# Performance work log

Measured on AMD Instinct MI355X. Metric: run time of the kernel, lower is better.

Reference implementation:

```python
import jax, jax.numpy as jnp
import numpy as np

DEPTH, HEADS, DIM, DH = 6, 3, 3, 128
INNER = HEADS * DH            # 384
M = int(DH * np.log(DH))      # 620 random features (performer_pytorch default)
FF = 4 * DIM                  # 12
EPS = 1e-4


def setup_inputs() -> dict:
    key = jax.random.key(0)
    ks = jax.random.split(key, 12)
    B, N = 8, 4096
    s = 0.1
    return {
        "x": jax.random.normal(ks[0], (B, N, DIM), jnp.float32),
        "Wq": jax.random.normal(ks[1], (DEPTH, DIM, INNER), jnp.float32) * s,
        "Wk": jax.random.normal(ks[2], (DEPTH, DIM, INNER), jnp.float32) * s,
        "Wv": jax.random.normal(ks[3], (DEPTH, DIM, INNER), jnp.float32) * s,
        "Wo": jax.random.normal(ks[4], (DEPTH, INNER, DIM), jnp.float32) * s,
        "bo": jnp.zeros((DEPTH, DIM), jnp.float32),
        "ln1_g": jnp.ones((DEPTH, DIM), jnp.float32),
        "ln1_b": jnp.zeros((DEPTH, DIM), jnp.float32),
        "W1": jax.random.normal(ks[5], (DEPTH, DIM, FF), jnp.float32) * s,
        "b1": jnp.zeros((DEPTH, FF), jnp.float32),
        "W2": jax.random.normal(ks[6], (DEPTH, FF, DIM), jnp.float32) * s,
        "b2": jnp.zeros((DEPTH, DIM), jnp.float32),
        "ln2_g": jnp.ones((DEPTH, DIM), jnp.float32),
        "ln2_b": jnp.zeros((DEPTH, DIM), jnp.float32),
        "proj": jax.random.normal(ks[7], (DEPTH, M, DH), jnp.float32),
        "dec_w": jax.random.normal(ks[8], (DIM, 1), jnp.float32) * s,
        "dec_b": jnp.zeros((1,), jnp.float32),
    }


def layernorm(x, g, b):
    mu = x.mean(-1, keepdims=True)
    var = ((x - mu) ** 2).mean(-1, keepdims=True)
    return (x - mu) * jax.lax.rsqrt(var + 1e-5) * g + b


def softmax_kernel(data, proj, is_query):
    # data: [b,h,n,dh], proj: [m,dh] -> positive random features [b,h,n,m]
    dn = DH ** -0.25                    # data normalizer 1/sqrt(sqrt(d))
    ratio = M ** -0.5
    dd = jnp.einsum('bhnd,md->bhnm', data * dn, proj)
    diag = 0.5 * (dn ** 2) * (data ** 2).sum(-1, keepdims=True)  # [b,h,n,1]
    if is_query:
        mx = jnp.max(dd, axis=-1, keepdims=True)
    else:
        mx = jnp.max(dd, axis=(-1, -2), keepdims=True)
    return ratio * (jnp.exp(dd - diag - mx) + EPS)


def favor_attention(x, Wq, Wk, Wv, Wo, bo, proj):
    b, n, _ = x.shape
    split = lambda t: t.reshape(b, n, HEADS, DH).transpose(0, 2, 1, 3)
    q, k, v = split(x @ Wq), split(x @ Wk), split(x @ Wv)   # [b,h,n,dh]
    qp = softmax_kernel(q, proj, True)    # [b,h,n,m]
    kp = softmax_kernel(k, proj, False)
    k_sum = kp.sum(axis=2)                                   # [b,h,m]
    d_inv = 1.0 / jnp.einsum('bhnm,bhm->bhn', qp, k_sum)
    ctx = jnp.einsum('bhnm,bhnd->bhmd', kp, v)               # [b,h,m,dh]
    out = jnp.einsum('bhnm,bhmd,bhn->bhnd', qp, ctx, d_inv)
    out = out.transpose(0, 2, 1, 3).reshape(b, n, INNER)
    return out @ Wo + bo


def reference(x, Wq, Wk, Wv, Wo, bo, ln1_g, ln1_b, W1, b1, W2, b2, ln2_g, ln2_b, proj, dec_w, dec_b):
    for i in range(DEPTH):
        h = layernorm(x, ln1_g[i], ln1_b[i])
        x = x + favor_attention(h, Wq[i], Wk[i], Wv[i], Wo[i], bo[i], proj[i])
        h = layernorm(x, ln2_g[i], ln2_b[i])
        x = x + (jax.nn.gelu(h @ W1[i] + b1[i], approximate=False) @ W2[i] + b2[i])
    return jax.nn.sigmoid(x @ dec_w + dec_b)
```

## Files before the change

kernel.cpp:

```cpp
#include <hip/hip_runtime.h>
#include <math.h>

#define B_ 8
#define N_ 4096
#define H_ 3
#define DH_ 128
#define INNER_ 384
#define M_ 620
#define MP_ 640
#define DEPTH_ 6
#define BH_ 24

static constexpr float DN_ = 0.29730177875068026f;
static constexpr float RATIO_ = 0.04016096644512494f;
static constexpr float EPS_ = 1e-4f;

typedef __attribute__((ext_vector_type(8))) short short8;
typedef __attribute__((ext_vector_type(4))) float f32x4;

__device__ __forceinline__ short f2bf(float f) {
  union { float f; unsigned u; } x; x.f = f;
  unsigned r = x.u + 0x7FFF + ((x.u >> 16) & 1);
  return (short)(r >> 16);
}
__device__ __forceinline__ float bf2f(short s) {
  union { unsigned u; float f; } x; x.u = ((unsigned)(unsigned short)s) << 16;
  return x.f;
}
__device__ __forceinline__ float4 ldg4(const float* p) { return *(const float4*)p; }

__device__ __forceinline__ unsigned cvtpk(float lo, float hi) {
  unsigned r;
  asm("v_cvt_pk_bf16_f32 %0, %1, %2" : "=v"(r) : "v"(lo), "v"(hi));
  return r;
}

__device__ __forceinline__ void gl2lds(const void* g, void* l) {
  __builtin_amdgcn_global_load_lds(
      (const __attribute__((address_space(1))) void*)g,
      (__attribute__((address_space(3))) void*)l, 16, 0, 0);
}

__device__ __forceinline__ void stage_t256(const char* gbase, char* lds, int w, int l) {
  int row = w * 4 + (l >> 4);
  int col = ((l & 15) * 16) ^ ((row & 7) << 4);
  char* lp = lds + __builtin_amdgcn_readfirstlane(w << 10);
  gl2lds(gbase + row * 256 + col, lp);
}

__device__ __forceinline__ void stage_t64(const char* gbase, size_t growb, char* lds,
                                          int w, int l) {
  int d = w * 16 + (l >> 2);
  int swl = ((((l >> 2) ^ (l >> 4)) & 3) << 4);
  int col = ((l & 3) * 16) ^ swl;
  char* lp = lds + __builtin_amdgcn_readfirstlane(w << 10);
  gl2lds(gbase + (size_t)d * growb + col, lp);
}

__global__ void k_copy(const float* __restrict__ s, float* __restrict__ d, int n) {
  int i = blockIdx.x * 256 + threadIdx.x;
  if (i < n) d[i] = s[i];
}

__global__ void k_projcvt(const float* __restrict__ proj, short* __restrict__ pb) {
  int i = blockIdx.x * 256 + threadIdx.x;
  if (i >= DEPTH_ * MP_ * DH_) return;
  int l = i / (MP_ * DH_);
  int rem = i - l * (MP_ * DH_);
  int m = rem >> 7, d = rem & 127;
  pb[i] = (m < M_) ? f2bf(proj[((size_t)l * M_ + m) * DH_ + d]) : (short)0;
}

__global__ __launch_bounds__(384) void k_ln_qkv(
    const float* __restrict__ x, const float* __restrict__ Wq,
    const float* __restrict__ Wk, const float* __restrict__ Wv,
    const float* __restrict__ g1, const float* __restrict__ b1,
    short* __restrict__ qb, short* __restrict__ kb, short* __restrict__ vtp) {
  __shared__ float xs[96];
  int c = threadIdx.x;
  int token0 = blockIdx.x * 32;
  int b = token0 >> 12, n0 = token0 & 4095;
  if (c < 96) xs[c] = x[(size_t)token0 * 3 + c];
  float wq0 = Wq[c], wq1 = Wq[INNER_ + c], wq2 = Wq[2 * INNER_ + c];
  float wk0 = Wk[c], wk1 = Wk[INNER_ + c], wk2 = Wk[2 * INNER_ + c];
  float wv0 = Wv[c], wv1 = Wv[INNER_ + c], wv2 = Wv[2 * INNER_ + c];
  float G0 = g1[0], G1 = g1[1], G2 = g1[2];
  float B0 = b1[0], B1 = b1[1], B2 = b1[2];
  int hh = c >> 7, dh = c & 127;
  size_t rowbase = ((size_t)(b * H_ + hh) * N_ + n0) * DH_ + dh;
  __syncthreads();
  short8 v8[4];
#pragma unroll
  for (int tt = 0; tt < 32; ++tt) {
    float x0 = xs[tt * 3], x1 = xs[tt * 3 + 1], x2 = xs[tt * 3 + 2];
    float mu = (x0 + x1 + x2) * (1.f / 3.f);
    float d0 = x0 - mu, d1 = x1 - mu, d2 = x2 - mu;
    float rs = rsqrtf((d0 * d0 + d1 * d1 + d2 * d2) * (1.f / 3.f) + 1e-5f);
    float h0 = d0 * rs * G0 + B0;
    float h1 = d1 * rs * G1 + B1;
    float h2 = d2 * rs * G2 + B2;
    qb[rowbase + (size_t)tt * DH_] = f2bf((h0 * wq0 + h1 * wq1 + h2 * wq2) * DN_);
    kb[rowbase + (size_t)tt * DH_] = f2bf((h0 * wk0 + h1 * wk1 + h2 * wk2) * DN_);
    const int p = ((tt >> 2) & 3) * 8 + ((tt >> 4) & 1) * 4 + (tt & 3);
    v8[p >> 3][p & 7] = f2bf(h0 * wv0 + h1 * wv1 + h2 * wv2);
  }
  short* dst = vtp + ((size_t)(b * H_ + hh) * DH_ + dh) * N_ + n0;
  *(short8*)dst = v8[0];
  *(short8*)(dst + 8) = v8[1];
  *(short8*)(dst + 16) = v8[2];
  *(short8*)(dst + 24) = v8[3];
}

__global__ __launch_bounds__(256) void k_diag(const short* __restrict__ kb,
                                              float* __restrict__ diag_k) {
  int nt = blockIdx.x, bh = blockIdx.y;
  int t = threadIdx.x;
  int n = t >> 3, seg = t & 7;
  const short* src = kb + ((size_t)bh * N_ + nt * 32 + n) * DH_ + seg * 16;
  short8 a = *(const short8*)src;
  short8 b2 = *(const short8*)(src + 8);
  float s = 0.f;
#pragma unroll
  for (int j = 0; j < 8; ++j) {
    float va = bf2f(a[j]), vb = bf2f(b2[j]);
    s = fmaf(va, va, s);
    s = fmaf(vb, vb, s);
  }
  s += __shfl_down(s, 4);
  s += __shfl_down(s, 2);
  s += __shfl_down(s, 1);
  if (seg == 0) diag_k[(size_t)bh * N_ + nt * 32 + n] = 0.5f * s;
}

__global__ __launch_bounds__(512) void k_kp_ctx(
    const short* __restrict__ kb, const short* __restrict__ vtp,
    const short* __restrict__ pb, const float* __restrict__ diag_k,
    float* __restrict__ Cpart, float* __restrict__ spart,
    float* __restrict__ bmx) {
  int ns = blockIdx.x, mt = blockIdx.y, bh = blockIdx.z;
  __shared__ __align__(16) char Ks[2][8192];
  __shared__ __align__(16) char Vts[2][8192];
  __shared__ float diag_s[1024];
  int t = threadIdx.x, w = t >> 6, l = t & 63, lr = l & 15, lg = l >> 4;
  {
    const float* dbase = diag_k + (size_t)bh * N_ + ns * 1024;
#pragma unroll
    for (int i = 0; i < 2; ++i) diag_s[t + i * 512] = dbase[t + i * 512];
  }
  int m0 = mt * 128 + w * 16;
  short8 bfr[4];
  {
    const short* pr = pb + (size_t)(m0 + lr) * DH_ + lg * 8;
#pragma unroll
    for (int ks = 0; ks < 4; ++ks) bfr[ks] = *(const short8*)(pr + ks * 32);
  }
  const char* kgb = (const char*)(kb + ((size_t)bh * N_ + ns * 1024) * DH_);
  const char* vgb = (const char*)(vtp + (size_t)bh * DH_ * N_ + ns * 1024);
  stage_t256(kgb, Ks[0], w, l);
  stage_t64(vgb, (size_t)N_ * 2, Vts[0], w, l);
  __syncthreads();
  f32x4 cacc[8];
#pragma unroll
  for (int db = 0; db < 8; ++db) cacc[db] = (f32x4){0.f, 0.f, 0.f, 0.f};
  float ksacc = 0.f;
  float bm = -INFINITY;
  const bool mv = (m0 + lr) < M_;
  int xk = (lr & 7) << 4;
  int xv = ((lr ^ (lr >> 2)) & 3) << 4;
  for (int ch = 0; ch < 32; ++ch) {
    int cur = ch & 1;
    if (ch < 31) {
      stage_t256(kgb + (size_t)(ch + 1) * 32 * 256, Ks[cur ^ 1], w, l);
      stage_t64(vgb + (size_t)(ch + 1) * 64, (size_t)N_ * 2, Vts[cur ^ 1], w, l);
    }
    int n0 = ch * 32;
    f32x4 dd[2];
    __builtin_amdgcn_s_setprio(1);
#pragma unroll
    for (int nsub = 0; nsub < 2; ++nsub) {
      f32x4 acc = {0.f, 0.f, 0.f, 0.f};
#pragma unroll
      for (int ks = 0; ks < 4; ++ks)
        acc = __builtin_amdgcn_mfma_f32_16x16x32_bf16(
            *(const short8*)(Ks[cur] + (nsub * 16 + lr) * 256 +
                             ((lg * 16 + ks * 64) ^ xk)),
            bfr[ks], acc, 0, 0, 0);
      dd[nsub] = acc;
    }
    __builtin_amdgcn_s_setprio(0);
    float cm = -INFINITY;
    if (mv) {
#pragma unroll
      for (int nsub = 0; nsub < 2; ++nsub)
#pragma unroll
        for (int rg = 0; rg < 4; ++rg) cm = fmaxf(cm, dd[nsub][rg]);
    }
#pragma unroll
    for (int off = 1; off < 64; off <<= 1) cm = fmaxf(cm, __shfl_xor(cm, off));
    if (cm > bm) {
      float sc = __expf(bm - cm);
      bm = cm;
      ksacc *= sc;
#pragma unroll
      for (int db = 0; db < 8; ++db)
#pragma unroll
        for (int rg = 0; rg < 4; ++rg) cacc[db][rg] *= sc;
    }
    float ev[8];
#pragma unroll
    for (int nsub = 0; nsub < 2; ++nsub)
#pragma unroll
      for (int rg = 0; rg < 4; ++rg) {
        float e = __expf(dd[nsub][rg] - diag_s[n0 + nsub * 16 + 4 * lg + rg] - bm);
        ev[nsub * 4 + rg] = e;
        ksacc += e;
      }
    union { short8 s8; unsigned u[4]; } ea;
#pragma unroll
    for (int i = 0; i < 4; ++i) ea.u[i] = cvtpk(ev[2 * i], ev[2 * i + 1]);
    __builtin_amdgcn_s_setprio(1);
#pragma unroll
    for (int db = 0; db < 8; ++db)
      cacc[db] = __builtin_amdgcn_mfma_f32_16x16x32_bf16(
          ea.s8, *(const short8*)(Vts[cur] + (db * 16 + lr) * 64 + ((lg * 16) ^ xv)),
          cacc[db], 0, 0, 0);
    __builtin_amdgcn_s_setprio(0);
    __syncthreads();
  }
  float* Cp = Cpart + ((size_t)ns * BH_ + bh) * MP_ * DH_;
#pragma unroll
  for (int db = 0; db < 8; ++db) {
    int d = db * 16 + lr;
#pragma unroll
    for (int rg = 0; rg < 4; ++rg)
      Cp[(size_t)(m0 + 4 * lg + rg) * DH_ + d] = cacc[db][rg];
  }
  ksacc += __shfl_down(ksacc, 32);
  ksacc += __shfl_down(ksacc, 16);
  if (l < 16) spart[((size_t)ns * BH_ + bh) * MP_ + m0 + l] = ksacc;
  if (l == 0) bmx[((size_t)ns * BH_ + bh) * 40 + mt * 8 + w] = bm;
}

__global__ __launch_bounds__(256) void k_gmax(const float* __restrict__ bmx,
                                              float* __restrict__ mxk) {
  int bh = blockIdx.x, t = threadIdx.x;
  float v = -INFINITY;
  if (t < 160) {
    int ns = t / 40, g = t - ns * 40;
    v = bmx[((size_t)ns * BH_ + bh) * 40 + g];
  }
#pragma unroll
  for (int off = 32; off; off >>= 1) v = fmaxf(v, __shfl_xor(v, off));
  __shared__ float red[4];
  if ((t & 63) == 0) red[t >> 6] = v;
  __syncthreads();
  if (t == 0) mxk[bh] = fmaxf(fmaxf(red[0], red[1]), fmaxf(red[2], red[3]));
}

__global__ __launch_bounds__(256) void k_vsum(
    const short* __restrict__ vtp, float* __restrict__ vsp) {
  int d = blockIdx.x, bh = blockIdx.y, t = threadIdx.x;
  const short8* row = (const short8*)(vtp + ((size_t)bh * DH_ + d) * N_);
  short8 a = row[t * 2], b2 = row[t * 2 + 1];
  float s = 0.f;
#pragma unroll
  for (int j = 0; j < 8; ++j) s += bf2f(a[j]) + bf2f(b2[j]);
  __shared__ float red[256];
  red[t] = s;
  __syncthreads();
  for (int st = 128; st; st >>= 1) {
    if (t < st) red[t] += red[t + st];
    __syncthreads();
  }
  if (t == 0) vsp[bh * DH_ + d] = red[0];
}

__global__ __launch_bounds__(256) void k_fin_ctx(
    const float* __restrict__ Cpart, const float* __restrict__ vsp,
    const float* __restrict__ bmx, const float* __restrict__ mxk,
    short* __restrict__ ctxtp, float* __restrict__ cspart) {
  int mt = blockIdx.x, bh = blockIdx.y;
  __shared__ float vsv[128];
  __shared__ short tile[128][40];
  int t = threadIdx.x;
  if (t < 128) vsv[t] = vsp[bh * DH_ + t] * EPS_;
  __syncthreads();
  int r = t >> 3, seg = t & 7;
  int d0 = seg * 16;
  int m = mt * 32 + r;
  int p = ((r >> 2) & 3) * 8 + ((r >> 4) & 1) * 4 + (r & 3);
  const size_t ph = (size_t)BH_ * MP_ * DH_;
  const float* c0 = Cpart + (size_t)bh * MP_ * DH_ + (size_t)m * DH_ + d0;
  if (m < M_) {
    float mxg = mxk[bh];
    int g = m >> 4;
    float sc0 = __expf(bmx[((size_t)0 * BH_ + bh) * 40 + g] - mxg);
    float sc1 = __expf(bmx[((size_t)1 * BH_ + bh) * 40 + g] - mxg);
    float sc2 = __expf(bmx[((size_t)2 * BH_ + bh) * 40 + g] - mxg);
    float sc3 = __expf(bmx[((size_t)3 * BH_ + bh) * 40 + g] - mxg);
#pragma unroll
    for (int j4 = 0; j4 < 4; ++j4) {
      float4 a = ldg4(c0 + j4 * 4);
      float4 b = ldg4(c0 + ph + j4 * 4);
      float4 c = ldg4(c0 + 2 * ph + j4 * 4);
      float4 e = ldg4(c0 + 3 * ph + j4 * 4);
      float vals[4] = {sc0 * a.x + sc1 * b.x + sc2 * c.x + sc3 * e.x,
                       sc0 * a.y + sc1 * b.y + sc2 * c.y + sc3 * e.y,
                       sc0 * a.z + sc1 * b.z + sc2 * c.z + sc3 * e.z,
                       sc0 * a.w + sc1 * b.w + sc2 * c.w + sc3 * e.w};
#pragma unroll
      for (int j = 0; j < 4; ++j) {
        int d = d0 + j4 * 4 + j;
        tile[d][p] = f2bf(RATIO_ * (vals[j] + vsv[d]));
      }
    }
  } else {
#pragma unroll
    for (int j = 0; j < 16; ++j) tile[d0 + j][p] = 0;
  }
  __syncthreads();
  int d = t >> 1, half = t & 1;
  short* dst = ctxtp + ((size_t)bh * DH_ + d) * MP_ + mt * 32 + half * 16;
  short8 s0 = *(const short8*)&tile[d][half * 16];
  short8 s1 = *(const short8*)&tile[d][half * 16 + 8];
  *(short8*)dst = s0;
  *(short8*)(dst + 8) = s1;
  float cs = 0.f;
#pragma unroll
  for (int j = 0; j < 8; ++j) cs += bf2f(s0[j]) + bf2f(s1[j]);
  cs += __shfl_xor(cs, 1);
  if (half == 0) cspart[((size_t)bh * 20 + mt) * DH_ + d] = cs;
}

__global__ __launch_bounds__(128) void k_fin2(
    const float* __restrict__ cspart, const float* __restrict__ spart,
    const float* __restrict__ bmx, const float* __restrict__ mxk,
    float* __restrict__ ctxsum, short* __restrict__ ksum_pb,
    float* __restrict__ ksumtot) {
  int bh = blockIdx.x, d = threadIdx.x;
  float s = 0.f;
#pragma unroll
  for (int mt = 0; mt < 20; ++mt) s += cspart[((size_t)bh * 20 + mt) * DH_ + d];
  ctxsum[bh * DH_ + d] = s;
  float mxg = mxk[bh];
  __shared__ float red[128];
  float kt = 0.f;
  for (int m = d; m < MP_; m += 128) {
    float ks = 0.f;
    if (m < M_) {
      size_t o = (size_t)bh * MP_ + m;
      size_t sh = (size_t)BH_ * MP_;
      int g = m >> 4;
      float s0 = __expf(bmx[((size_t)0 * BH_ + bh) * 40 + g] - mxg);
      float s1 = __expf(bmx[((size_t)1 * BH_ + bh) * 40 + g] - mxg);
      float s2 = __expf(bmx[((size_t)2 * BH_ + bh) * 40 + g] - mxg);
      float s3 = __expf(bmx[((size_t)3 * BH_ + bh) * 40 + g] - mxg);
      ks = RATIO_ * (s0 * spart[o] + s1 * spart[o + sh] + s2 * spart[o + 2 * sh] +
                     s3 * spart[o + 3 * sh] + EPS_ * (float)N_);
    }
    int r = m & 31;
    int p = ((r >> 2) & 3) * 8 + ((r >> 4) & 1) * 4 + (r & 3);
    ksum_pb[(size_t)bh * MP_ + (m & ~31) + p] = f2bf(ks);
    kt += ks;
  }
  red[d] = kt;
  __syncthreads();
  for (int st = 64; st > 0; st >>= 1) {
    if (d < st) red[d] += red[d + st];
    __syncthreads();
  }
  if (d == 0) ksumtot[bh] = red[0];
}

__global__ __launch_bounds__(512) void k_q_attn(
    const short* __restrict__ qb, const short* __restrict__ pb,
    const short* __restrict__ ctxtp, const short* __restrict__ ksum_pb,
    const float* __restrict__ ctxsum, const float* __restrict__ ksumtot,
    float* __restrict__ o) {
  int nt = blockIdx.x, bh = blockIdx.y;
  __shared__ __align__(16) char Pj[2][8192];
  __shared__ __align__(16) char Ct[2][8192];
  __shared__ __align__(16) short kslp[MP_];
  int t = threadIdx.x, w = t >> 6, l = t & 63, lr = l & 15, lg = l >> 4;
  if (t < MP_ / 8)
    ((short8*)kslp)[t] = ((const short8*)(ksum_pb + (size_t)bh * MP_))[t];
  const short* qr = qb + ((size_t)bh * N_ + nt * 128 + w * 16 + lr) * DH_ + lg * 8;
  short8 qfr[4];
#pragma unroll
  for (int ks = 0; ks < 4; ++ks) qfr[ks] = *(const short8*)(qr + ks * 32);
  float dq;
  {
    float s2 = 0.f;
#pragma unroll
    for (int ks = 0; ks < 4; ++ks)
#pragma unroll
      for (int j = 0; j < 8; ++j) {
        float v = bf2f(qfr[ks][j]);
        s2 = fmaf(v, v, s2);
      }
    s2 += __shfl_xor(s2, 16);
    s2 += __shfl_xor(s2, 32);
    dq = 0.5f * s2;
  }
  const char* cgb = (const char*)(ctxtp + (size_t)bh * DH_ * MP_);
  stage_t256((const char*)pb, Pj[0], w, l);
  stage_t64(cgb, (size_t)MP_ * 2, Ct[0], w, l);
  __syncthreads();
  f32x4 cacc[8];
#pragma unroll
  for (int db = 0; db < 8; ++db) cacc[db] = (f32x4){0.f, 0.f, 0.f, 0.f};
  f32x4 dacc = {0.f, 0.f, 0.f, 0.f};
  float om = -INFINITY;
  int xk = (lr & 7) << 4;
  int xv = ((lr ^ (lr >> 2)) & 3) << 4;
  for (int mc = 0; mc < 20; ++mc) {
    int cur = mc & 1;
    if (mc < 19) {
      stage_t256((const char*)(pb + (size_t)(mc + 1) * 32 * DH_), Pj[cur ^ 1], w, l);
      stage_t64(cgb + (size_t)(mc + 1) * 64, (size_t)MP_ * 2, Ct[cur ^ 1], w, l);
    }
    int m0 = mc * 32;
    f32x4 qk[2];
    __builtin_amdgcn_s_setprio(1);
#pragma unroll
    for (int ms = 0; ms < 2; ++ms) {
      f32x4 acc = {0.f, 0.f, 0.f, 0.f};
#pragma unroll
      for (int ks = 0; ks < 4; ++ks)
        acc = __builtin_amdgcn_mfma_f32_16x16x32_bf16(
            *(const short8*)(Pj[cur] + (ms * 16 + lr) * 256 +
                             ((lg * 16 + ks * 64) ^ xk)),
            qfr[ks], acc, 0, 0, 0);
      qk[ms] = acc;
    }
    __builtin_amdgcn_s_setprio(0);
    float cm = -INFINITY;
#pragma unroll
    for (int ms = 0; ms < 2; ++ms)
#pragma unroll
      for (int rg = 0; rg < 4; ++rg) {
        int mg = m0 + ms * 16 + 4 * lg + rg;
        if (mg < M_) cm = fmaxf(cm, qk[ms][rg]);
      }
    cm = fmaxf(cm, __shfl_xor(cm, 16));
    cm = fmaxf(cm, __shfl_xor(cm, 32));
    if (__any(cm > om)) {
      float nm = fmaxf(om, cm);
      float sc = __expf(om - nm);
      om = nm;
      float scr[4];
#pragma unroll
      for (int rg = 0; rg < 4; ++rg) scr[rg] = __shfl(sc, 4 * lg + rg);
#pragma unroll
      for (int rg = 0; rg < 4; ++rg) dacc[rg] *= scr[rg];
#pragma unroll
      for (int db = 0; db < 8; ++db)
#pragma unroll
        for (int rg = 0; rg < 4; ++rg) cacc[db][rg] *= scr[rg];
    }
    float dqm = dq + om;
    float ev[8];
#pragma unroll
    for (int ms = 0; ms < 2; ++ms)
#pragma unroll
      for (int rg = 0; rg < 4; ++rg)
        ev[ms * 4 + rg] = __expf(qk[ms][rg] - dqm);
    union { short8 s8; unsigned u[4]; } ea;
#pragma unroll
    for (int i = 0; i < 4; ++i) ea.u[i] = cvtpk(ev[2 * i], ev[2 * i + 1]);
    __builtin_amdgcn_s_setprio(1);
    dacc = __builtin_amdgcn_mfma_f32_16x16x32_bf16(
        ea.s8, *(const short8*)&kslp[m0 + lg * 8], dacc, 0, 0, 0);
#pragma unroll
    for (int db = 0; db < 8; ++db)
      cacc[db] = __builtin_amdgcn_mfma_f32_16x16x32_bf16(
          ea.s8, *(const short8*)(Ct[cur] + (db * 16 + lr) * 64 + ((lg * 16) ^ xv)),
          cacc[db], 0, 0, 0);
    __builtin_amdgcn_s_setprio(0);
    __syncthreads();
  }
  float kst = ksumtot[bh];
  float dinv[4];
#pragma unroll
  for (int rg = 0; rg < 4; ++rg)
    dinv[rg] = 1.f / (RATIO_ * (dacc[rg] + EPS_ * kst));
  float* ob = o + ((size_t)bh * N_ + nt * 128 + w * 16) * DH_;
#pragma unroll
  for (int db = 0; db < 8; ++db) {
    int d = db * 16 + lr;
    float cs = ctxsum[bh * DH_ + d] * EPS_;
#pragma unroll
    for (int rg = 0; rg < 4; ++rg)
      ob[(size_t)(4 * lg + rg) * DH_ + d] = RATIO_ * (cacc[db][rg] + cs) * dinv[rg];
  }
}

__global__ __launch_bounds__(256) void k_wo_ffn(
    const float* __restrict__ attn, const float* __restrict__ Wo,
    const float* __restrict__ bo, const float* __restrict__ g2,
    const float* __restrict__ be2, const float* __restrict__ W1,
    const float* __restrict__ bf1, const float* __restrict__ W2,
    const float* __restrict__ bf2, float* __restrict__ x) {
  __shared__ float wols[INNER_ * 3];
  __shared__ float bos[3];
  __shared__ float acc3[4][8][3];
  int t = threadIdx.x;
  for (int i = t; i < INNER_ * 3; i += 256) wols[i] = Wo[i];
  if (t < 3) bos[t] = bo[t];
  __syncthreads();
  int w = t >> 6, l = t & 63;
  int base = (blockIdx.x * 4 + w) * 8;
#pragma unroll
  for (int tt = 0; tt < 8; ++tt) {
    int token = base + tt;
    int b = token >> 12, n = token & 4095;
    float p0 = 0.f, p1 = 0.f, p2 = 0.f;
#pragma unroll
    for (int s = 0; s < 6; ++s) {
      int inner = l + 64 * s;
      int h = inner >> 7, dh = inner & 127;
      float a = attn[(((size_t)(b * H_ + h)) * N_ + n) * DH_ + dh];
      p0 = fmaf(a, wols[inner * 3 + 0], p0);
      p1 = fmaf(a, wols[inner * 3 + 1], p1);
      p2 = fmaf(a, wols[inner * 3 + 2], p2);
    }
#pragma unroll
    for (int off = 32; off; off >>= 1) {
      p0 += __shfl_down(p0, off);
      p1 += __shfl_down(p1, off);
      p2 += __shfl_down(p2, off);
    }
    if (l == 0) {
      acc3[w][tt][0] = p0 + bos[0];
      acc3[w][tt][1] = p1 + bos[1];
      acc3[w][tt][2] = p2 + bos[2];
    }
  }
  __syncthreads();
  if (l < 8) {
    int token = base + l;
    float x0 = x[(size_t)token * 3 + 0] + acc3[w][l][0];
    float x1 = x[(size_t)token * 3 + 1] + acc3[w][l][1];
    float x2 = x[(size_t)token * 3 + 2] + acc3[w][l][2];
    float mu = (x0 + x1 + x2) * (1.f / 3.f);
    float d0 = x0 - mu, d1 = x1 - mu, d2 = x2 - mu;
    float rs = rsqrtf((d0 * d0 + d1 * d1 + d2 * d2) * (1.f / 3.f) + 1e-5f);
    float h0 = d0 * rs * g2[0] + be2[0];
    float h1 = d1 * rs * g2[1] + be2[1];
    float h2 = d2 * rs * g2[2] + be2[2];
    float y0 = x0 + bf2[0], y1 = x1 + bf2[1], y2 = x2 + bf2[2];
#pragma unroll
    for (int tt = 0; tt < 12; ++tt) {
      float f = h0 * W1[tt] + h1 * W1[12 + tt] + h2 * W1[24 + tt] + bf1[tt];
      float g = 0.5f * f * (1.f + erff(f * 0.70710678118654752f));
      y0 += g * W2[tt * 3 + 0];
      y1 += g * W2[tt * 3 + 1];
      y2 += g * W2[tt * 3 + 2];
    }
    x[(size_t)token * 3 + 0] = y0;
    x[(size_t)token * 3 + 1] = y1;
    x[(size_t)token * 3 + 2] = y2;
  }
}

__global__ void k_decode(const float* __restrict__ x, const float* __restrict__ dw,
                         const float* __restrict__ db, float* __restrict__ out) {
  int t = blockIdx.x * 256 + threadIdx.x;
  if (t < B_ * N_) {
    float l = x[(size_t)t * 3 + 0] * dw[0] + x[(size_t)t * 3 + 1] * dw[1] +
              x[(size_t)t * 3 + 2] * dw[2] + db[0];
    out[t] = 1.f / (1.f + expf(-l));
  }
}

extern "C" void kernel_launch(void* const* d_in, const int* in_sizes, int n_in,
                              void* d_out, int out_size, void* d_ws, size_t ws_size,
                              hipStream_t stream) {
  const float* x_in = (const float*)d_in[0];
  const float* Wq = (const float*)d_in[1];
  const float* Wk = (const float*)d_in[2];
  const float* Wv = (const float*)d_in[3];
  const float* Wo = (const float*)d_in[4];
  const float* bo = (const float*)d_in[5];
  const float* ln1g = (const float*)d_in[6];
  const float* ln1b = (const float*)d_in[7];
  const float* W1 = (const float*)d_in[8];
  const float* b1 = (const float*)d_in[9];
  const float* W2 = (const float*)d_in[10];
  const float* b2 = (const float*)d_in[11];
  const float* ln2g = (const float*)d_in[12];
  const float* ln2b = (const float*)d_in[13];
  const float* proj = (const float*)d_in[14];
  const float* dec_w = (const float*)d_in[15];
  const float* dec_b = (const float*)d_in[16];

  const size_t XB = (size_t)B_ * N_ * 3;
  const size_t QKV = (size_t)BH_ * N_ * DH_;
  const size_t CTX = (size_t)BH_ * MP_ * DH_;
  const size_t SS = (size_t)BH_ * MP_;

  char* p = (char*)d_ws;
  auto alloc = [&](size_t bytes) {
    char* r = p;
    p += (bytes + 255) & ~(size_t)255;
    return r;
  };
  float* xbuf = (float*)alloc(XB * 4);
  short* qb = (short*)alloc(QKV * 2);
  short* kb = (short*)alloc(QKV * 2);
  float* diag_k = (float*)alloc((size_t)BH_ * N_ * 4);
  short* pb = (short*)alloc((size_t)DEPTH_ * MP_ * DH_ * 2);
  short* vtp = (short*)alloc(QKV * 2);
  short* ctxtp = (short*)alloc(CTX * 2);
  float* o = (float*)alloc(QKV * 4);
  float* Cpart = o;
  float* spart = (float*)alloc(4 * SS * 4);
  float* cspart = (float*)alloc((size_t)BH_ * 20 * DH_ * 4);
  short* ksum_pb = (short*)alloc(SS * 2);
  float* vsp = (float*)alloc((size_t)BH_ * DH_ * 4);
  float* ctxsum = (float*)alloc((size_t)BH_ * DH_ * 4);
  float* ksumtot = (float*)alloc(BH_ * 4);
  float* bmx = (float*)alloc((size_t)4 * BH_ * 40 * 4);
  float* mxk = (float*)alloc(BH_ * 4);

  k_copy<<<(XB + 255) / 256, 256, 0, stream>>>(x_in, xbuf, (int)XB);
  k_projcvt<<<(DEPTH_ * MP_ * DH_ + 255) / 256, 256, 0, stream>>>(proj, pb);

  for (int i = 0; i < DEPTH_; ++i) {
    const short* pbL = pb + (size_t)i * MP_ * DH_;
    k_ln_qkv<<<B_ * N_ / 32, 384, 0, stream>>>(xbuf, Wq + (size_t)i * 3 * INNER_,
                                               Wk + (size_t)i * 3 * INNER_,
                                               Wv + (size_t)i * 3 * INNER_,
                                               ln1g + i * 3, ln1b + i * 3,
                                               qb, kb, vtp);
    k_diag<<<dim3(N_ / 32, BH_), 256, 0, stream>>>(kb, diag_k);
    k_kp_ctx<<<dim3(4, 5, BH_), 512, 0, stream>>>(kb, vtp, pbL, diag_k,
                                                  Cpart, spart, bmx);
    k_vsum<<<dim3(DH_, BH_), 256, 0, stream>>>(vtp, vsp);
    k_gmax<<<BH_, 256, 0, stream>>>(bmx, mxk);
    k_fin_ctx<<<dim3(20, BH_), 256, 0, stream>>>(Cpart, vsp, bmx, mxk,
                                                 ctxtp, cspart);
    k_fin2<<<BH_, 128, 0, stream>>>(cspart, spart, bmx, mxk,
                                    ctxsum, ksum_pb, ksumtot);
    k_q_attn<<<dim3(32, BH_), 512, 0, stream>>>(qb, pbL, ctxtp, ksum_pb,
                                                ctxsum, ksumtot, o);
    k_wo_ffn<<<B_ * N_ / 32, 256, 0, stream>>>(o, Wo + (size_t)i * INNER_ * 3,
                                               bo + i * 3, ln2g + i * 3, ln2b + i * 3,
                                               W1 + (size_t)i * 36, b1 + (size_t)i * 12,
                                               W2 + (size_t)i * 36, b2 + i * 3, xbuf);
  }
  k_decode<<<(B_ * N_ + 255) / 256, 256, 0, stream>>>(xbuf, dec_w, dec_b, (float*)d_out);
}
```

Before: 1.075 ms.

## Merge diag/vsum kernels, fold gmax into finalizers, double k_kp_ctx stage size

Merges the k_diag and k_vsum kernels into one launch that branches on blockIdx. The k_gmax kernel is removed and its per-head max reduction is recomputed inside both k_fin_ctx and k_fin2. k_kp_ctx now stages 64 rows per pipeline step instead of 32, halving the number of barriers and loop iterations at the cost of twice the shared memory (about 68KB), which may reduce occupancy. The main aim is to cut launch overhead and synchronisation across six layers.

New measurement: 1.044 ms. 1.03x faster.

```diff
diff --git a/kernel.cpp b/kernel.cpp
--- a/kernel.cpp
+++ b/kernel.cpp
@@ -111,25 +111,43 @@
   *(short8*)(dst + 24) = v8[3];
 }
 
-__global__ __launch_bounds__(256) void k_diag(const short* __restrict__ kb,
-                                              float* __restrict__ diag_k) {
-  int nt = blockIdx.x, bh = blockIdx.y;
-  int t = threadIdx.x;
-  int n = t >> 3, seg = t & 7;
-  const short* src = kb + ((size_t)bh * N_ + nt * 32 + n) * DH_ + seg * 16;
-  short8 a = *(const short8*)src;
-  short8 b2 = *(const short8*)(src + 8);
-  float s = 0.f;
-#pragma unroll
-  for (int j = 0; j < 8; ++j) {
-    float va = bf2f(a[j]), vb = bf2f(b2[j]);
-    s = fmaf(va, va, s);
-    s = fmaf(vb, vb, s);
-  }
-  s += __shfl_down(s, 4);
-  s += __shfl_down(s, 2);
-  s += __shfl_down(s, 1);
-  if (seg == 0) diag_k[(size_t)bh * N_ + nt * 32 + n] = 0.5f * s;
+__global__ __launch_bounds__(256) void k_dv(
+    const short* __restrict__ kb, const short* __restrict__ vtp,
+    float* __restrict__ diag_k, float* __restrict__ vsp) {
+  __shared__ float red[256];
+  int xx = blockIdx.x, bh = blockIdx.y, t = threadIdx.x;
+  if (xx < 128) {
+    int d = xx;
+    const short8* row = (const short8*)(vtp + ((size_t)bh * DH_ + d) * N_);
+    short8 a = row[t * 2], b2 = row[t * 2 + 1];
+    float s = 0.f;
+#pragma unroll
+    for (int j = 0; j < 8; ++j) s += bf2f(a[j]) + bf2f(b2[j]);
+    red[t] = s;
+    __syncthreads();
+    for (int st = 128; st; st >>= 1) {
+      if (t < st) red[t] += red[t + st];
+      __syncthreads();
+    }
+    if (t == 0) vsp[bh * DH_ + d] = red[0];
+  } else {
+    int nt = xx - 128;
+    int n = t >> 3, seg = t & 7;
+    const short* src = kb + ((size_t)bh * N_ + nt * 32 + n) * DH_ + seg * 16;
+    short8 a = *(const short8*)src;
+    short8 b2 = *(const short8*)(src + 8);
+    float s = 0.f;
+#pragma unroll
+    for (int j = 0; j < 8; ++j) {
+      float va = bf2f(a[j]), vb = bf2f(b2[j]);
+      s = fmaf(va, va, s);
+      s = fmaf(vb, vb, s);
+    }
+    s += __shfl_down(s, 4);
+    s += __shfl_down(s, 2);
+    s += __shfl_down(s, 1);
+    if (seg == 0) diag_k[(size_t)bh * N_ + nt * 32 + n] = 0.5f * s;
+  }
 }
 
 __global__ __launch_bounds__(512) void k_kp_ctx(
@@ -138,8 +156,8 @@
     float* __restrict__ Cpart, float* __restrict__ spart,
     float* __restrict__ bmx) {
   int ns = blockIdx.x, mt = blockIdx.y, bh = blockIdx.z;
-  __shared__ __align__(16) char Ks[2][8192];
-  __shared__ __align__(16) char Vts[2][8192];
+  __shared__ __align__(16) char Ks[2][16384];
+  __shared__ __align__(16) char Vts[2][16384];
   __shared__ float diag_s[1024];
   int t = threadIdx.x, w = t >> 6, l = t & 63, lr = l & 15, lg = l >> 4;
   {
@@ -157,7 +175,9 @@
   const char* kgb = (const char*)(kb + ((size_t)bh * N_ + ns * 1024) * DH_);
   const char* vgb = (const char*)(vtp + (size_t)bh * DH_ * N_ + ns * 1024);
   stage_t256(kgb, Ks[0], w, l);
+  stage_t256(kgb + 32 * 256, Ks[0] + 8192, w, l);
   stage_t64(vgb, (size_t)N_ * 2, Vts[0], w, l);
+  stage_t64(vgb + 64, (size_t)N_ * 2, Vts[0] + 8192, w, l);
   __syncthreads();
   f32x4 cacc[8];
 #pragma unroll
@@ -167,64 +187,73 @@
   const bool mv = (m0 + lr) < M_;
   int xk = (lr & 7) << 4;
   int xv = ((lr ^ (lr >> 2)) & 3) << 4;
-  for (int ch = 0; ch < 32; ++ch) {
-    int cur = ch & 1;
-    if (ch < 31) {
-      stage_t256(kgb + (size_t)(ch + 1) * 32 * 256, Ks[cur ^ 1], w, l);
-      stage_t64(vgb + (size_t)(ch + 1) * 64, (size_t)N_ * 2, Vts[cur ^ 1], w, l);
-    }
-    int n0 = ch * 32;
-    f32x4 dd[2];
-    __builtin_amdgcn_s_setprio(1);
-#pragma unroll
-    for (int nsub = 0; nsub < 2; ++nsub) {
-      f32x4 acc = {0.f, 0.f, 0.f, 0.f};
-#pragma unroll
-      for (int ks = 0; ks < 4; ++ks)
-        acc = __builtin_amdgcn_mfma_f32_16x16x32_bf16(
-            *(const short8*)(Ks[cur] + (nsub * 16 + lr) * 256 +
-                             ((lg * 16 + ks * 64) ^ xk)),
-            bfr[ks], acc, 0, 0, 0);
-      dd[nsub] = acc;
-    }
-    __builtin_amdgcn_s_setprio(0);
-    float cm = -INFINITY;
-    if (mv) {
+  for (int pc = 0; pc < 16; ++pc) {
+    int cur = pc & 1;
+    if (pc < 15) {
+      const char* kc = kgb + (size_t)(2 * pc + 2) * 32 * 256;
+      stage_t256(kc, Ks[cur ^ 1], w, l);
+      stage_t256(kc + 32 * 256, Ks[cur ^ 1] + 8192, w, l);
+      const char* vc = vgb + (size_t)(2 * pc + 2) * 64;
+      stage_t64(vc, (size_t)N_ * 2, Vts[cur ^ 1], w, l);
+      stage_t64(vc + 64, (size_t)N_ * 2, Vts[cur ^ 1] + 8192, w, l);
+    }
+#pragma unroll
+    for (int sub = 0; sub < 2; ++sub) {
+      const char* KS = Ks[cur] + sub * 8192;
+      const char* VS = Vts[cur] + sub * 8192;
+      int n0 = (2 * pc + sub) * 32;
+      f32x4 dd[2];
+      __builtin_amdgcn_s_setprio(1);
+#pragma unroll
+      for (int nsub = 0; nsub < 2; ++nsub) {
+        f32x4 acc = {0.f, 0.f, 0.f, 0.f};
+#pragma unroll
+        for (int ks = 0; ks < 4; ++ks)
+          acc = __builtin_amdgcn_mfma_f32_16x16x32_bf16(
+              *(const short8*)(KS + (nsub * 16 + lr) * 256 +
+                               ((lg * 16 + ks * 64) ^ xk)),
+              bfr[ks], acc, 0, 0, 0);
+        dd[nsub] = acc;
+      }
+      __builtin_amdgcn_s_setprio(0);
+      float cm = -INFINITY;
+      if (mv) {
+#pragma unroll
+        for (int nsub = 0; nsub < 2; ++nsub)
+#pragma unroll
+          for (int rg = 0; rg < 4; ++rg) cm = fmaxf(cm, dd[nsub][rg]);
+      }
+#pragma unroll
+      for (int off = 1; off < 64; off <<= 1) cm = fmaxf(cm, __shfl_xor(cm, off));
+      if (cm > bm) {
+        float sc = __expf(bm - cm);
+        bm = cm;
+        ksacc *= sc;
+#pragma unroll
+        for (int db = 0; db < 8; ++db)
+#pragma unroll
+          for (int rg = 0; rg < 4; ++rg) cacc[db][rg] *= sc;
+      }
+      float ev[8];
 #pragma unroll
       for (int nsub = 0; nsub < 2; ++nsub)
 #pragma unroll
-        for (int rg = 0; rg < 4; ++rg) cm = fmaxf(cm, dd[nsub][rg]);
-    }
-#pragma unroll
-    for (int off = 1; off < 64; off <<= 1) cm = fmaxf(cm, __shfl_xor(cm, off));
-    if (cm > bm) {
-      float sc = __expf(bm - cm);
-      bm = cm;
-      ksacc *= sc;
+        for (int rg = 0; rg < 4; ++rg) {
+          float e = __expf(dd[nsub][rg] - diag_s[n0 + nsub * 16 + 4 * lg + rg] - bm);
+          ev[nsub * 4 + rg] = e;
+          ksacc += e;
+        }
+      union { short8 s8; unsigned u[4]; } ea;
+#pragma unroll
+      for (int i = 0; i < 4; ++i) ea.u[i] = cvtpk(ev[2 * i], ev[2 * i + 1]);
+      __builtin_amdgcn_s_setprio(1);
 #pragma unroll
       for (int db = 0; db < 8; ++db)
-#pragma unroll
-        for (int rg = 0; rg < 4; ++rg) cacc[db][rg] *= sc;
-    }
-    float ev[8];
-#pragma unroll
-    for (int nsub = 0; nsub < 2; ++nsub)
-#pragma unroll
-      for (int rg = 0; rg < 4; ++rg) {
-        float e = __expf(dd[nsub][rg] - diag_s[n0 + nsub * 16 + 4 * lg + rg] - bm);
-        ev[nsub * 4 + rg] = e;
-        ksacc += e;
-      }
-    union { short8 s8; unsigned u[4]; } ea;
-#pragma unroll
-    for (int i = 0; i < 4; ++i) ea.u[i] = cvtpk(ev[2 * i], ev[2 * i + 1]);
-    __builtin_amdgcn_s_setprio(1);
-#pragma unroll
-    for (int db = 0; db < 8; ++db)
-      cacc[db] = __builtin_amdgcn_mfma_f32_16x16x32_bf16(
-          ea.s8, *(const short8*)(Vts[cur] + (db * 16 + lr) * 64 + ((lg * 16) ^ xv)),
-          cacc[db], 0, 0, 0);
-    __builtin_amdgcn_s_setprio(0);
+        cacc[db] = __builtin_amdgcn_mfma_f32_16x16x32_bf16(
+            ea.s8, *(const short8*)(VS + (db * 16 + lr) * 64 + ((lg * 16) ^ xv)),
+            cacc[db], 0, 0, 0);
+      __builtin_amdgcn_s_setprio(0);
+    }
     __syncthreads();
   }
   float* Cp = Cpart + ((size_t)ns * BH_ + bh) * MP_ * DH_;
@@ -241,50 +270,26 @@
   if (l == 0) bmx[((size_t)ns * BH_ + bh) * 40 + mt * 8 + w] = bm;
 }
 
-__global__ __launch_bounds__(256) void k_gmax(const float* __restrict__ bmx,
-                                              float* __restrict__ mxk) {
-  int bh = blockIdx.x, t = threadIdx.x;
-  float v = -INFINITY;
-  if (t < 160) {
-    int ns = t / 40, g = t - ns * 40;
-    v = bmx[((size_t)ns * BH_ + bh) * 40 + g];
-  }
-#pragma unroll
-  for (int off = 32; off; off >>= 1) v = fmaxf(v, __shfl_xor(v, off));
-  __shared__ float red[4];
-  if ((t & 63) == 0) red[t >> 6] = v;
-  __syncthreads();
-  if (t == 0) mxk[bh] = fmaxf(fmaxf(red[0], red[1]), fmaxf(red[2], red[3]));
-}
-
-__global__ __launch_bounds__(256) void k_vsum(
-    const short* __restrict__ vtp, float* __restrict__ vsp) {
-  int d = blockIdx.x, bh = blockIdx.y, t = threadIdx.x;
-  const short8* row = (const short8*)(vtp + ((size_t)bh * DH_ + d) * N_);
-  short8 a = row[t * 2], b2 = row[t * 2 + 1];
-  float s = 0.f;
-#pragma unroll
-  for (int j = 0; j < 8; ++j) s += bf2f(a[j]) + bf2f(b2[j]);
-  __shared__ float red[256];
-  red[t] = s;
-  __syncthreads();
-  for (int st = 128; st; st >>= 1) {
-    if (t < st) red[t] += red[t + st];
-    __syncthreads();
-  }
-  if (t == 0) vsp[bh * DH_ + d] = red[0];
-}
-
 __global__ __launch_bounds__(256) void k_fin_ctx(
     const float* __restrict__ Cpart, const float* __restrict__ vsp,
-    const float* __restrict__ bmx, const float* __restrict__ mxk,
+    const float* __restrict__ bmx,
     short* __restrict__ ctxtp, float* __restrict__ cspart) {
   int mt = blockIdx.x, bh = blockIdx.y;
   __shared__ float vsv[128];
   __shared__ short tile[128][40];
+  __shared__ float redm[4];
   int t = threadIdx.x;
   if (t < 128) vsv[t] = vsp[bh * DH_ + t] * EPS_;
-  __syncthreads();
+  float v = -INFINITY;
+  if (t < 160) {
+    int nsg = t / 40, g = t - nsg * 40;
+    v = bmx[((size_t)nsg * BH_ + bh) * 40 + g];
+  }
+#pragma unroll
+  for (int off = 32; off; off >>= 1) v = fmaxf(v, __shfl_xor(v, off));
+  if ((t & 63) == 0) redm[t >> 6] = v;
+  __syncthreads();
+  float mxg = fmaxf(fmaxf(redm[0], redm[1]), fmaxf(redm[2], redm[3]));
   int r = t >> 3, seg = t & 7;
   int d0 = seg * 16;
   int m = mt * 32 + r;
@@ -292,7 +297,6 @@
   const size_t ph = (size_t)BH_ * MP_ * DH_;
   const float* c0 = Cpart + (size_t)bh * MP_ * DH_ + (size_t)m * DH_ + d0;
   if (m < M_) {
-    float mxg = mxk[bh];
     int g = m >> 4;
     float sc0 = __expf(bmx[((size_t)0 * BH_ + bh) * 40 + g] - mxg);
     float sc1 = __expf(bmx[((size_t)1 * BH_ + bh) * 40 + g] - mxg);
@@ -334,15 +338,25 @@
 
 __global__ __launch_bounds__(128) void k_fin2(
     const float* __restrict__ cspart, const float* __restrict__ spart,
-    const float* __restrict__ bmx, const float* __restrict__ mxk,
+    const float* __restrict__ bmx,
     float* __restrict__ ctxsum, short* __restrict__ ksum_pb,
     float* __restrict__ ksumtot) {
   int bh = blockIdx.x, d = threadIdx.x;
+  __shared__ float redm[2];
+  float v = -INFINITY;
+  for (int i = d; i < 160; i += 128) {
+    int nsg = i / 40, g = i - nsg * 40;
+    v = fmaxf(v, bmx[((size_t)nsg * BH_ + bh) * 40 + g]);
+  }
+#pragma unroll
+  for (int off = 32; off; off >>= 1) v = fmaxf(v, __shfl_xor(v, off));
+  if ((d & 63) == 0) redm[d >> 6] = v;
   float s = 0.f;
 #pragma unroll
   for (int mt = 0; mt < 20; ++mt) s += cspart[((size_t)bh * 20 + mt) * DH_ + d];
   ctxsum[bh * DH_ + d] = s;
-  float mxg = mxk[bh];
+  __syncthreads();
+  float mxg = fmaxf(redm[0], redm[1]);
   __shared__ float red[128];
   float kt = 0.f;
   for (int m = d; m < MP_; m += 128) {
@@ -621,7 +635,6 @@
   float* ctxsum = (float*)alloc((size_t)BH_ * DH_ * 4);
   float* ksumtot = (float*)alloc(BH_ * 4);
   float* bmx = (float*)alloc((size_t)4 * BH_ * 40 * 4);
-  float* mxk = (float*)alloc(BH_ * 4);
 
   k_copy<<<(XB + 255) / 256, 256, 0, stream>>>(x_in, xbuf, (int)XB);
   k_projcvt<<<(DEPTH_ * MP_ * DH_ + 255) / 256, 256, 0, stream>>>(proj, pb);
@@ -633,15 +646,11 @@
                                                Wv + (size_t)i * 3 * INNER_,
                                                ln1g + i * 3, ln1b + i * 3,
                                                qb, kb, vtp);
-    k_diag<<<dim3(N_ / 32, BH_), 256, 0, stream>>>(kb, diag_k);
+    k_dv<<<dim3(256, BH_), 256, 0, stream>>>(kb, vtp, diag_k, vsp);
     k_kp_ctx<<<dim3(4, 5, BH_), 512, 0, stream>>>(kb, vtp, pbL, diag_k,
                                                   Cpart, spart, bmx);
-    k_vsum<<<dim3(DH_, BH_), 256, 0, stream>>>(vtp, vsp);
-    k_gmax<<<BH_, 256, 0, stream>>>(bmx, mxk);
-    k_fin_ctx<<<dim3(20, BH_), 256, 0, stream>>>(Cpart, vsp, bmx, mxk,
-                                                 ctxtp, cspart);
-    k_fin2<<<BH_, 128, 0, stream>>>(cspart, spart, bmx, mxk,
-                                    ctxsum, ksum_pb, ksumtot);
+    k_fin_ctx<<<dim3(20, BH_), 256, 0, stream>>>(Cpart, vsp, bmx, ctxtp, cspart);
+    k_fin2<<<BH_, 128, 0, stream>>>(cspart, spart, bmx, ctxsum, ksum_pb, ksumtot);
     k_q_attn<<<dim3(32, BH_), 512, 0, stream>>>(qb, pbL, ctxtp, ksum_pb,
                                                 ctxsum, ksumtot, o);
     k_wo_ffn<<<B_ * N_ / 32, 256, 0, stream>>>(o, Wo + (size_t)i * INNER_ * 3,
```
